# Kernel tuning notes

Measured on AMD Instinct MI355X. Metric: run time of the kernel, lower is better.

## Reference

```python
import jax, jax.numpy as jnp
import numpy as np

IMG = 512; P = 16; C = 3; DIM = 512; DEPTH = 2; HEADS = 8; HD = DIM // HEADS
MLP = 2048; W = 64; NCLS = 1000; B = 8
NPATCH = (IMG // P) ** 2          # 1024
N0 = NPATCH + 1                    # 1025 tokens incl CLS
PAD = (-N0) % (2 * W)              # pad to multiple of 2w (sliding_chunks)
N = N0 + PAD                       # 1152


def _ln(x, w, b):
    m = x.mean(-1, keepdims=True)
    v = jnp.mean((x - m) ** 2, -1, keepdims=True)
    return (x - m) * jax.lax.rsqrt(v + 1e-5) * w + b


def _heads(t):
    b, n, _ = t.shape
    return t.reshape(b, n, HEADS, HD).transpose(0, 2, 1, 3)  # b h n d


def _attn(x, mask, wq, bq, wk, bk, wv, bv, wqg, bqg, wkg, bkg, wvg, bvg):
    b, n, _ = x.shape
    sc = 1.0 / np.sqrt(HD)
    q = _heads(x @ wq + bq) * sc
    k = _heads(x @ wk + bk)
    v = _heads(x @ wv + bv)
    nc = n // W
    qc = q.reshape(b, HEADS, nc, W, HD)

    def chunk3(t):  # gather prev/self/next chunk of keys/values: b h nc 3W d
        tc = t.reshape(b, HEADS, nc, W, HD)
        z = jnp.zeros_like(tc[:, :, :1])
        prev = jnp.concatenate([z, tc[:, :, :-1]], 2)
        nxt = jnp.concatenate([tc[:, :, 1:], z], 2)
        return jnp.concatenate([prev, tc, nxt], 3)

    k3, v3 = chunk3(k), chunk3(v)
    band = jnp.einsum('bhcqd,bhckd->bhcqk', qc, k3)  # b h nc W 3W
    qi = jnp.arange(W)[:, None]
    kk = jnp.arange(3 * W)[None, :]
    rel_ok = jnp.abs(kk - W - qi) <= W               # exact +-w band
    kglob = jnp.arange(nc)[:, None, None] * W + (kk - W)[None]  # nc 1 3W
    in_rng = (kglob >= 0) & (kglob < n)
    kmask = mask[jnp.clip(kglob, 0, n - 1)]
    # keep only real local keys: exclude pad (0) and global (2, handled by gcol)
    keep = rel_ok[None] & in_rng & (kmask == 1.0)    # nc W 3W
    band = jnp.where(keep[None, None], band, -1e9)
    gcol = jnp.einsum('bhnd,bhd->bhn', q, k[:, :, 0])  # attend to global CLS key
    scores = jnp.concatenate([gcol[..., None], band.reshape(b, HEADS, n, 3 * W)], -1)
    a = jax.nn.softmax(scores, -1)                   # b h n (1+3W)
    out = jnp.einsum('bhcqk,bhckd->bhcqd', a[..., 1:].reshape(b, HEADS, nc, W, 3 * W), v3)
    out = out.reshape(b, HEADS, n, HD) + a[..., 0:1] * v[:, :, 0:1]
    # global CLS row attends to everything with its own projections
    qg0 = ((x[:, 0] @ wqg + bqg) * sc).reshape(b, HEADS, HD)
    kg = _heads(x @ wkg + bkg)
    vg = _heads(x @ wvg + bvg)
    gs = jnp.where(mask[None, None] > 0, jnp.einsum('bhd,bhnd->bhn', qg0, kg), -1e9)
    gout = jnp.einsum('bhn,bhnd->bhd', jax.nn.softmax(gs, -1), vg)
    out = out.at[:, :, 0].set(gout)
    return out.transpose(0, 2, 1, 3).reshape(b, n, DIM)


def setup_inputs():
    key = jax.random.key(0)
    ks = iter(jax.random.split(key, 20))

    def w(shape, s=0.02):
        return jax.random.normal(next(ks), shape, jnp.float32) * s

    return {
        'img': jax.random.normal(next(ks), (B, C, IMG, IMG), jnp.float32),
        'patch_w': w((P * P * C, DIM)), 'patch_b': jnp.zeros((DIM,), jnp.float32),
        'cls_tok': jax.random.uniform(next(ks), (1, 1, DIM), jnp.float32),
        'pos_emb': w((1, N0, DIM), 1.0),
        'ln1_w': jnp.ones((DEPTH, DIM), jnp.float32), 'ln1_b': jnp.zeros((DEPTH, DIM), jnp.float32),
        'wq': w((DEPTH, DIM, DIM)), 'bq': jnp.zeros((DEPTH, DIM), jnp.float32),
        'wk': w((DEPTH, DIM, DIM)), 'bk': jnp.zeros((DEPTH, DIM), jnp.float32),
        'wv': w((DEPTH, DIM, DIM)), 'bv': jnp.zeros((DEPTH, DIM), jnp.float32),
        'wqg': w((DEPTH, DIM, DIM)), 'bqg': jnp.zeros((DEPTH, DIM), jnp.float32),
        'wkg': w((DEPTH, DIM, DIM)), 'bkg': jnp.zeros((DEPTH, DIM), jnp.float32),
        'wvg': w((DEPTH, DIM, DIM)), 'bvg': jnp.zeros((DEPTH, DIM), jnp.float32),
        'ln2_w': jnp.ones((DEPTH, DIM), jnp.float32), 'ln2_b': jnp.zeros((DEPTH, DIM), jnp.float32),
        'w1': w((DEPTH, DIM, MLP)), 'b1': jnp.zeros((DEPTH, MLP), jnp.float32),
        'w2': w((DEPTH, MLP, DIM)), 'b2': jnp.zeros((DEPTH, DIM), jnp.float32),
        'head_ln_w': jnp.ones((DIM,), jnp.float32), 'head_ln_b': jnp.zeros((DIM,), jnp.float32),
        'head_w': w((DIM, NCLS)), 'head_b': jnp.zeros((NCLS,), jnp.float32),
    }


def reference(img, patch_w, patch_b, cls_tok, pos_emb, ln1_w, ln1_b, wq, bq, wk, bk,
              wv, bv, wqg, bqg, wkg, bkg, wvg, bvg, ln2_w, ln2_b, w1, b1, w2, b2,
              head_ln_w, head_ln_b, head_w, head_b):
    b = img.shape[0]
    hh = IMG // P
    # b c (h p1) (w p2) -> b (h w) (p1 p2 c)
    x = img.reshape(b, C, hh, P, hh, P).transpose(0, 2, 4, 3, 5, 1).reshape(b, hh * hh, P * P * C)
    x = x @ patch_w + patch_b
    x = jnp.concatenate([jnp.broadcast_to(cls_tok, (b, 1, DIM)), x], 1) + pos_emb
    x = jnp.pad(x, ((0, 0), (0, PAD), (0, 0)))
    mask = jnp.zeros((N,), jnp.float32).at[:N0].set(1.0).at[0].set(2.0)
    for i in range(DEPTH):
        x = x + _attn(_ln(x, ln1_w[i], ln1_b[i]), mask,
                      wq[i], bq[i], wk[i], bk[i], wv[i], bv[i],
                      wqg[i], bqg[i], wkg[i], bkg[i], wvg[i], bvg[i])
        h = jax.nn.gelu(_ln(x, ln2_w[i], ln2_b[i]) @ w1[i] + b1[i], approximate=False)
        x = x + h @ w2[i] + b2[i]
    cls = x[:, 0]  # pool='cls'
    return _ln(cls, head_ln_w, head_ln_b) @ head_w + head_b
```

## Files before the change

kernel.cpp:

```cpp
#include <hip/hip_runtime.h>
#include <hip/hip_bf16.h>
#include <math.h>

typedef __hip_bfloat16 bf16;
typedef float f32x4 __attribute__((ext_vector_type(4)));
typedef short s16x8 __attribute__((ext_vector_type(8)));
typedef unsigned int u32;

#define NB 8
#define NROW 1025
#define MTOT (NB*NROW)
#define DIMD 512
#define NHEAD 8
#define HD 64
#define MLPD 2048
#define QKVN 2560
#define JSTR 1032

__device__ __forceinline__ float b2f(short u) {
    return __builtin_bit_cast(float, (u32)(unsigned short)u << 16);
}
__device__ __forceinline__ unsigned short f2bfbits(float f) {
    __hip_bfloat16 h = __float2bfloat16(f);
    return __builtin_bit_cast(unsigned short, h);
}
__device__ __forceinline__ void g2lds16(const bf16* g, bf16* l) {
    __builtin_amdgcn_global_load_lds((const __attribute__((address_space(1))) u32*)g,
                                     (__attribute__((address_space(3))) u32*)l, 16, 0, 0);
}

__global__ __launch_bounds__(256) void transpose_cvt_L(
    const float* __restrict__ src, bf16* __restrict__ dst, int K, int N, float scale)
{
    __shared__ float t[32][33];
    const int z = blockIdx.z;
    const float* s = src + (size_t)z * K * N;
    bf16* d = dst + (size_t)z * N * K;
    const int n0 = blockIdx.x * 32, k0 = blockIdx.y * 32;
    const int tx = threadIdx.x, ty = threadIdx.y;
#pragma unroll
    for (int i = 0; i < 32; i += 8)
        t[ty + i][tx] = s[(long)(k0 + ty + i) * N + n0 + tx];
    __syncthreads();
#pragma unroll
    for (int i = 0; i < 32; i += 8)
        d[(long)(n0 + ty + i) * K + k0 + tx] = __float2bfloat16(t[tx][ty + i] * scale);
}

__global__ __launch_bounds__(256) void qkvw_t(
    const float* __restrict__ wq, const float* __restrict__ wk, const float* __restrict__ wv,
    const float* __restrict__ wkg, const float* __restrict__ wvg, bf16* __restrict__ qkvT)
{
    __shared__ float t[32][33];
    const int z = blockIdx.z, L = z / 5, s = z % 5;
    const float* srcs[5] = {wq, wk, wv, wkg, wvg};
    const float* src = srcs[s] + (size_t)L * DIMD * DIMD;
    bf16* dst = qkvT + ((size_t)L * QKVN + s * DIMD) * DIMD;
    const float scale = (s == 0) ? 0.125f : 1.f;
    const int n0 = blockIdx.x * 32, k0 = blockIdx.y * 32;
    const int tx = threadIdx.x, ty = threadIdx.y;
#pragma unroll
    for (int i = 0; i < 32; i += 8)
        t[ty + i][tx] = src[(long)(k0 + ty + i) * DIMD + n0 + tx];
    __syncthreads();
#pragma unroll
    for (int i = 0; i < 32; i += 8)
        dst[(long)(n0 + ty + i) * DIMD + k0 + tx] = __float2bfloat16(t[tx][ty + i] * scale);
}

__global__ __launch_bounds__(256) void build_bias(
    const float* __restrict__ bq, const float* __restrict__ bk, const float* __restrict__ bv,
    const float* __restrict__ bkg, const float* __restrict__ bvg, float* __restrict__ outb)
{
    int idx = blockIdx.x * 256 + threadIdx.x;
    if (idx >= 2 * QKVN) return;
    int L = idx / QKVN, c = idx % QKVN;
    int sec = c >> 9, d = c & 511;
    const float* src = (sec == 0) ? bq : (sec == 1) ? bk : (sec == 2) ? bv : (sec == 3) ? bkg : bvg;
    float v = src[L * DIMD + d];
    if (sec == 0) v *= 0.125f;
    outb[idx] = v;
}

__global__ __launch_bounds__(256) void im2col(
    const float* __restrict__ img, bf16* __restrict__ A)
{
    long idx = (long)blockIdx.x * 256 + threadIdx.x;
    if (idx >= (long)NB * 3 * 512 * 128) return;
    int ww4 = idx & 127;
    int hh  = (int)((idx >> 7) & 511);
    long rem = idx >> 16;
    int c = (int)(rem % 3), b = (int)(rem / 3);
    int w = ww4 * 4;
    const float4 pix = *(const float4*)(img + (((long)(b * 3 + c) * 512 + hh) * 512 + w));
    int ph = hh >> 4, py = hh & 15;
    int pw = w >> 4, px0 = w & 15;
    long arow = (long)b * 1024 + ph * 32 + pw;
    long abase = arow * 768 + (py * 16) * 3 + c;
    A[abase + (px0 + 0) * 3] = __float2bfloat16(pix.x);
    A[abase + (px0 + 1) * 3] = __float2bfloat16(pix.y);
    A[abase + (px0 + 2) * 3] = __float2bfloat16(pix.z);
    A[abase + (px0 + 3) * 3] = __float2bfloat16(pix.w);
}

__global__ __launch_bounds__(256) void assemble(
    const float* __restrict__ po, const float* __restrict__ cls,
    const float* __restrict__ pos, float* __restrict__ x)
{
    long idx = (long)blockIdx.x * 256 + threadIdx.x;
    if (idx >= (long)NB * NROW * DIMD) return;
    int d = (int)(idx & 511);
    long rem = idx >> 9;
    int n = (int)(rem % NROW), b = (int)(rem / NROW);
    float v;
    if (n == 0) v = cls[d] + pos[d];
    else        v = po[((long)b * 1024 + (n - 1)) * DIMD + d] + pos[(long)n * DIMD + d];
    x[idx] = v;
}

__global__ __launch_bounds__(256) void ln_fwd(
    const float* __restrict__ x, const float* __restrict__ w,
    const float* __restrict__ bb, bf16* __restrict__ y, int Mrows)
{
    const int row = blockIdx.x * 4 + (threadIdx.x >> 6);
    if (row >= Mrows) return;
    const int lane = threadIdx.x & 63;
    const float* xr = x + (long)row * DIMD + lane * 8;
    float4 a = *(const float4*)xr;
    float4 b4 = *(const float4*)(xr + 4);
    float s  = a.x + a.y + a.z + a.w + b4.x + b4.y + b4.z + b4.w;
    float sq = a.x*a.x + a.y*a.y + a.z*a.z + a.w*a.w + b4.x*b4.x + b4.y*b4.y + b4.z*b4.z + b4.w*b4.w;
#pragma unroll
    for (int o = 32; o; o >>= 1) { s += __shfl_xor(s, o); sq += __shfl_xor(sq, o); }
    float mean = s * (1.f / 512.f);
    float rstd = rsqrtf(sq * (1.f / 512.f) - mean * mean + 1e-5f);
    bf16* yr = y + (long)row * DIMD + lane * 8;
    const float* wp = w + lane * 8;
    const float* bp = bb + lane * 8;
    float vals[8] = {a.x, a.y, a.z, a.w, b4.x, b4.y, b4.z, b4.w};
#pragma unroll
    for (int u = 0; u < 8; ++u)
        yr[u] = __float2bfloat16((vals[u] - mean) * rstd * wp[u] + bp[u]);
}

template<int EPI>
__global__ __launch_bounds__(256) void gemm128(
    const bf16* __restrict__ A, const bf16* __restrict__ Bt,
    const float* __restrict__ bias,
    float* __restrict__ Cf, bf16* __restrict__ Cb,
    int M, int N, int K)
{
    __shared__ bf16 aL[2][128 * 32];
    __shared__ bf16 bL[2][128 * 32];
    const int tid = threadIdx.x, lane = tid & 63, w = tid >> 6;
    const int m0 = blockIdx.y * 128, n0 = blockIdx.x * 128;
    const int wm = w >> 1, wn = w & 1;
    f32x4 acc[4][4] = {};
    const int nk = K >> 5;
    const int lrow = lane >> 2, lk = (lane & 3) * 8;

#define STAGE(buf, kt) do {                                                       \
        _Pragma("unroll")                                                         \
        for (int i = 0; i < 2; ++i) {                                             \
            const int chunk = i * 4 + w;                                          \
            const int row = chunk * 16 + lrow;                                    \
            long ar = m0 + row; if (ar >= M) ar = M - 1;                          \
            g2lds16(A  + ar * (long)K + (long)(kt) * 32 + lk, &aL[buf][chunk*512]);\
            g2lds16(Bt + (long)(n0 + row) * K + (long)(kt) * 32 + lk, &bL[buf][chunk*512]);\
        } } while (0)

    STAGE(0, 0);
    __syncthreads();
    int cur = 0;
    const int abase = (wm * 64 + (lane & 15)) * 32 + (lane >> 4) * 8;
    const int bbase = (wn * 64 + (lane & 15)) * 32 + (lane >> 4) * 8;
    for (int kt = 0; kt < nk; ++kt) {
        if (kt + 1 < nk) STAGE(cur ^ 1, kt + 1);
        s16x8 af[4], bf_[4];
#pragma unroll
        for (int mi = 0; mi < 4; ++mi) af[mi]  = *(const s16x8*)(&aL[cur][abase + mi * 512]);
#pragma unroll
        for (int ni = 0; ni < 4; ++ni) bf_[ni] = *(const s16x8*)(&bL[cur][bbase + ni * 512]);
#pragma unroll
        for (int mi = 0; mi < 4; ++mi)
#pragma unroll
            for (int ni = 0; ni < 4; ++ni)
                acc[mi][ni] = __builtin_amdgcn_mfma_f32_16x16x32_bf16(af[mi], bf_[ni], acc[mi][ni], 0, 0, 0);
        __syncthreads();
        cur ^= 1;
    }
#undef STAGE
    const int lr = (lane >> 4) * 4, lc = lane & 15;
#pragma unroll
    for (int mi = 0; mi < 4; ++mi) {
        const int gr0 = m0 + wm * 64 + mi * 16 + lr;
#pragma unroll
        for (int ni = 0; ni < 4; ++ni) {
            const int gc = n0 + wn * 64 + ni * 16 + lc;
            const float bv = bias[gc];
#pragma unroll
            for (int j = 0; j < 4; ++j) {
                const int gr = gr0 + j;
                if (gr < M) {
                    float v = acc[mi][ni][j] + bv;
                    if (EPI == 0) Cf[(long)gr * N + gc] = v;
                    else if (EPI == 1) Cb[(long)gr * N + gc] = __float2bfloat16(v);
                    else if (EPI == 2) {
                        float g = 0.5f * v * (1.f + erff(v * 0.70710678118f));
                        Cb[(long)gr * N + gc] = __float2bfloat16(g);
                    } else {
                        Cf[(long)gr * N + gc] += v;
                    }
                }
            }
        }
    }
}

__global__ __launch_bounds__(256) void transpose_v(
    const bf16* __restrict__ qkv, bf16* __restrict__ vT)
{
    __shared__ bf16 t[32][34];
    const int b = blockIdx.z;
    const int j0 = blockIdx.x * 32, d0 = blockIdx.y * 32;
    const int tx = threadIdx.x, ty = threadIdx.y;
#pragma unroll
    for (int i = 0; i < 32; i += 8) {
        int j = j0 + ty + i; if (j > 1024) j = 1024;
        t[ty + i][tx] = qkv[((long)b * NROW + j) * QKVN + 1024 + d0 + tx];
    }
    __syncthreads();
#pragma unroll
    for (int i = 0; i < 32; i += 8) {
        int j = j0 + tx;
        if (j <= 1024)
            vT[((long)b * 512 + d0 + ty + i) * JSTR + j] = t[tx][ty + i];
    }
}

__global__ __launch_bounds__(256) void band_attn_mfma(
    const bf16* __restrict__ qkv, const bf16* __restrict__ vT, float* __restrict__ x)
{
    __shared__ bf16 Kl[208 * 72];
    __shared__ bf16 Vt[64 * 192];
    __shared__ bf16 Pl[4 * 16 * 192];
    __shared__ float V0l[64];
    const int c = blockIdx.x, h = blockIdx.y, b = blockIdx.z;
    const int tid = threadIdx.x, lane = tid & 63, w = tid >> 6;
    const int qi0 = 1 + c * 64, jbase = qi0 - 64;
    const long rowb = (long)b * NROW;
    const int hoff = h * HD;

    for (int task = tid; task < 208 * 8; task += 256) {
        const int d8 = task & 7, r = task >> 3;
        s16x8 val = {};
        if (r <= 192) {
            int j = (r < 192) ? (jbase + r) : 0;
            j = j < 0 ? 0 : (j > 1024 ? 1024 : j);
            val = *(const s16x8*)(qkv + (rowb + j) * QKVN + 512 + hoff + d8 * 8);
        }
        *(s16x8*)(Kl + r * 72 + d8 * 8) = val;
    }
    for (int task = tid; task < 64 * 24; task += 256) {
        const int kc = task % 24, d = task / 24;
        int j0 = jbase + kc * 8;
        j0 = j0 < 0 ? 0 : (j0 > 1017 ? 1017 : j0);
        s16x8 v = *(const s16x8*)(vT + ((long)(b * 512 + hoff + d)) * JSTR + j0);
        const int bo = (d * 384 + kc * 16) ^ ((d & 7) << 4);
        *(s16x8*)((char*)Vt + bo) = v;
    }
    if (tid < 64) V0l[tid] = __bfloat162float(qkv[rowb * QKVN + 1024 + hoff + tid]);

    const int q = lane & 15, g = lane >> 4;
    const int qg = w * 16 + q;
    s16x8 qf0, qf1;
    {
        const bf16* qp = qkv + (rowb + qi0 + qg) * QKVN + hoff + g * 8;
        qf0 = *(const s16x8*)qp;
        qf1 = *(const s16x8*)(qp + 32);
    }
    __syncthreads();

    f32x4 sc[13] = {};
#pragma unroll
    for (int nt = 0; nt < 13; ++nt) {
        const bf16* kp = Kl + (nt * 16 + q) * 72 + g * 8;
        s16x8 k0 = *(const s16x8*)kp;
        s16x8 k1 = *(const s16x8*)(kp + 32);
        sc[nt] = __builtin_amdgcn_mfma_f32_16x16x32_bf16(k0, qf0, sc[nt], 0, 0, 0);
        sc[nt] = __builtin_amdgcn_mfma_f32_16x16x32_bf16(k1, qf1, sc[nt], 0, 0, 0);
    }

    const int lo_ = (qg > 1 - jbase) ? qg : 1 - jbase;
    const int hi_ = (qg + 128 < 1024 - jbase) ? qg + 128 : 1024 - jbase;
    float m = -1e30f;
#pragma unroll
    for (int nt = 0; nt < 12; ++nt)
#pragma unroll
        for (int j = 0; j < 4; ++j) {
            const int slot = nt * 16 + g * 4 + j;
            float s = (slot >= lo_ && slot <= hi_) ? sc[nt][j] : -1e9f;
            sc[nt][j] = s;
            m = fmaxf(m, s);
        }
#pragma unroll
    for (int j = 0; j < 4; ++j) {
        float s = (g == 0 && j == 0) ? sc[12][j] : -1e9f;
        sc[12][j] = s;
        m = fmaxf(m, s);
    }
    m = fmaxf(m, __shfl_xor(m, 16));
    m = fmaxf(m, __shfl_xor(m, 32));
    float sum = 0.f;
#pragma unroll
    for (int nt = 0; nt < 13; ++nt)
#pragma unroll
        for (int j = 0; j < 4; ++j) {
            float p = __expf(sc[nt][j] - m);
            sc[nt][j] = p;
            sum += p;
        }
    sum += __shfl_xor(sum, 16);
    sum += __shfl_xor(sum, 32);
    const float inv = 1.f / sum;
    const float a0 = __shfl(sc[12][0], q);

    char* plw = (char*)Pl + w * 6144;
#pragma unroll
    for (int nt = 0; nt < 12; ++nt) {
        u32 lo2 = (u32)f2bfbits(sc[nt][0]) | ((u32)f2bfbits(sc[nt][1]) << 16);
        u32 hi2 = (u32)f2bfbits(sc[nt][2]) | ((u32)f2bfbits(sc[nt][3]) << 16);
        const int bo = (q * 384 + (nt * 16 + g * 4) * 2) ^ ((q & 7) << 4);
        *(uint2*)(plw + bo) = make_uint2(lo2, hi2);
    }
    __syncthreads();

    f32x4 ac[4] = {};
#pragma unroll
    for (int ks = 0; ks < 6; ++ks) {
        const int pbo = (q * 384 + (ks * 32 + g * 8) * 2) ^ ((q & 7) << 4);
        s16x8 pf = *(const s16x8*)(plw + pbo);
#pragma unroll
        for (int mt = 0; mt < 4; ++mt) {
            const int d = mt * 16 + q;
            const int vbo = ((d * 192 + ks * 32 + g * 8) * 2) ^ ((d & 7) << 4);
            s16x8 vf = *(const s16x8*)((char*)Vt + vbo);
            ac[mt] = __builtin_amdgcn_mfma_f32_16x16x32_bf16(vf, pf, ac[mt], 0, 0, 0);
        }
    }

    float* xr = x + (rowb + qi0 + qg) * DIMD + hoff;
#pragma unroll
    for (int mt = 0; mt < 4; ++mt) {
        const int d0 = mt * 16 + g * 4;
        float4 prev = *(float4*)(xr + d0);
        prev.x += (ac[mt][0] + a0 * V0l[d0 + 0]) * inv;
        prev.y += (ac[mt][1] + a0 * V0l[d0 + 1]) * inv;
        prev.z += (ac[mt][2] + a0 * V0l[d0 + 2]) * inv;
        prev.w += (ac[mt][3] + a0 * V0l[d0 + 3]) * inv;
        *(float4*)(xr + d0) = prev;
    }
}

__global__ __launch_bounds__(256) void qg_proj(
    const bf16* __restrict__ ybf, const float* __restrict__ wqg,
    const float* __restrict__ bqg, float* __restrict__ qg_all)
{
    __shared__ float y0[512];
    const int b = blockIdx.x, tid = threadIdx.x;
    const long rowb = (long)b * NROW;
    for (int d = tid; d < 512; d += 256) y0[d] = __bfloat162float(ybf[rowb * DIMD + d]);
    __syncthreads();
    const int c = blockIdx.y * 256 + tid;
    float a = 0.f;
#pragma unroll 8
    for (int kk = 0; kk < 512; ++kk) a += y0[kk] * wqg[(long)kk * DIMD + c];
    qg_all[b * DIMD + c] = (a + bqg[c]) * 0.125f;
}

__global__ __launch_bounds__(256) void glob_av(
    const float* __restrict__ qg_all, const bf16* __restrict__ qkv, float* __restrict__ x)
{
    __shared__ float qgs[64];
    __shared__ float red[256];
    __shared__ float P[1025];
    const int hh = blockIdx.x, b = blockIdx.y;
    const int tid = threadIdx.x;
    const long rowb = (long)b * NROW;
    const int hoff = hh * HD;
    if (tid < 64) qgs[tid] = qg_all[b * DIMD + hoff + tid];
    __syncthreads();
    const int dd = tid & 63, part = tid >> 6;
    for (int j = tid; j < 1025; j += 256) {
        const bf16* kr = qkv + (rowb + j) * QKVN + 1536 + hoff;
        float s = 0.f;
#pragma unroll
        for (int c8 = 0; c8 < 8; ++c8) {
            s16x8 kv = *(const s16x8*)(kr + c8 * 8);
#pragma unroll
            for (int e = 0; e < 8; ++e) s += qgs[c8 * 8 + e] * b2f(kv[e]);
        }
        P[j] = s;
    }
    __syncthreads();
    float lm = -1e30f;
    for (int j = tid; j < 1025; j += 256) lm = fmaxf(lm, P[j]);
    red[tid] = lm; __syncthreads();
    for (int st = 128; st; st >>= 1) { if (tid < st) red[tid] = fmaxf(red[tid], red[tid + st]); __syncthreads(); }
    const float mx = red[0]; __syncthreads();
    float ls = 0.f;
    for (int j = tid; j < 1025; j += 256) { float e = __expf(P[j] - mx); P[j] = e; ls += e; }
    red[tid] = ls; __syncthreads();
    for (int st = 128; st; st >>= 1) { if (tid < st) red[tid] += red[tid + st]; __syncthreads(); }
    const float inv = 1.f / red[0];
    __syncthreads();
    float acc = 0.f;
#pragma unroll 4
    for (int j = part; j < 1025; j += 4)
        acc += P[j] * __bfloat162float(qkv[(rowb + j) * QKVN + 2048 + hoff + dd]);
    red[tid] = acc;
    __syncthreads();
    if (part == 0)
        x[rowb * DIMD + hoff + dd] += (red[dd] + red[64 + dd] + red[128 + dd] + red[192 + dd]) * inv;
}

__global__ __launch_bounds__(512) void lncls(
    const float* __restrict__ x, const float* __restrict__ lw,
    const float* __restrict__ lb, float* __restrict__ out)
{
    const int b = threadIdx.x >> 6, lane = threadIdx.x & 63;
    const int d0 = lane * 8;
    const float* xr = x + (long)b * NROW * DIMD + d0;
    float4 a = *(const float4*)xr;
    float4 b4 = *(const float4*)(xr + 4);
    float s  = a.x + a.y + a.z + a.w + b4.x + b4.y + b4.z + b4.w;
    float sq = a.x*a.x + a.y*a.y + a.z*a.z + a.w*a.w + b4.x*b4.x + b4.y*b4.y + b4.z*b4.z + b4.w*b4.w;
#pragma unroll
    for (int o = 32; o; o >>= 1) { s += __shfl_xor(s, o); sq += __shfl_xor(sq, o); }
    const float mean = s * (1.f / 512.f);
    const float rstd = rsqrtf(sq * (1.f / 512.f) - mean * mean + 1e-5f);
    float vals[8] = {a.x, a.y, a.z, a.w, b4.x, b4.y, b4.z, b4.w};
#pragma unroll
    for (int u = 0; u < 8; ++u)
        out[b * DIMD + d0 + u] = (vals[u] - mean) * rstd * lw[d0 + u] + lb[d0 + u];
}

__global__ __launch_bounds__(128) void head_gemv(
    const float* __restrict__ lnc, const float* __restrict__ hw,
    const float* __restrict__ hb, float* __restrict__ out)
{
    const int idx = blockIdx.x * 128 + threadIdx.x;
    if (idx >= NB * 1000) return;
    const int b = idx / 1000, cc = idx - b * 1000;
    const float* lr = lnc + b * DIMD;
    float a = hb[cc];
#pragma unroll 8
    for (int kk = 0; kk < 512; ++kk) a += lr[kk] * hw[(long)kk * 1000 + cc];
    out[idx] = a;
}

extern "C" void kernel_launch(void* const* d_in, const int* in_sizes, int n_in,
                              void* d_out, int out_size, void* d_ws, size_t ws_size,
                              hipStream_t stream)
{
    const float* img     = (const float*)d_in[0];
    const float* patch_w = (const float*)d_in[1];
    const float* patch_b = (const float*)d_in[2];
    const float* cls_tok = (const float*)d_in[3];
    const float* pos_emb = (const float*)d_in[4];
    const float* ln1_w   = (const float*)d_in[5];
    const float* ln1_b   = (const float*)d_in[6];
    const float* wq  = (const float*)d_in[7];
    const float* bq  = (const float*)d_in[8];
    const float* wk  = (const float*)d_in[9];
    const float* bk  = (const float*)d_in[10];
    const float* wv  = (const float*)d_in[11];
    const float* bv  = (const float*)d_in[12];
    const float* wqg = (const float*)d_in[13];
    const float* bqg = (const float*)d_in[14];
    const float* wkg = (const float*)d_in[15];
    const float* bkg = (const float*)d_in[16];
    const float* wvg = (const float*)d_in[17];
    const float* bvg = (const float*)d_in[18];
    const float* ln2_w = (const float*)d_in[19];
    const float* ln2_b = (const float*)d_in[20];
    const float* w1 = (const float*)d_in[21];
    const float* b1 = (const float*)d_in[22];
    const float* w2 = (const float*)d_in[23];
    const float* b2 = (const float*)d_in[24];
    const float* hlw = (const float*)d_in[25];
    const float* hlb = (const float*)d_in[26];
    const float* hw  = (const float*)d_in[27];
    const float* hb  = (const float*)d_in[28];

    char* wsb = (char*)d_ws;
    size_t o = 0;
    auto carve = [&](size_t n) { size_t r = o; o += (n + 255) & ~(size_t)255; return r; };
    float* x    = (float*)(wsb + carve((size_t)MTOT * DIMD * 4));
    bf16*  ybf  = (bf16*) (wsb + carve((size_t)MTOT * DIMD * 2));
    bf16*  qkv  = (bf16*) (wsb + carve((size_t)MTOT * QKVN * 2));
    bf16*  hbuf = (bf16*) (wsb + carve((size_t)MTOT * MLPD * 2));
    float* pout = (float*)(wsb + carve((size_t)8192 * DIMD * 4));
    bf16*  acol = (bf16*) (wsb + carve((size_t)8192 * 768 * 2));
    bf16*  pwt  = (bf16*) (wsb + carve((size_t)512 * 768 * 2));
    bf16*  qkvT = (bf16*) (wsb + carve((size_t)2 * QKVN * DIMD * 2));
    bf16*  w1t  = (bf16*) (wsb + carve((size_t)2 * MLPD * DIMD * 2));
    bf16*  w2t  = (bf16*) (wsb + carve((size_t)2 * DIMD * MLPD * 2));
    float* catb = (float*)(wsb + carve((size_t)2 * QKVN * 4));
    float* qg_all = (float*)(wsb + carve((size_t)NB * DIMD * 4));
    float* lnc    = (float*)(wsb + carve((size_t)NB * DIMD * 4));
    bf16*  vT   = (bf16*)pout;
    (void)ws_size; (void)in_sizes; (void)n_in; (void)out_size;

    dim3 tb(32, 8);
    transpose_cvt_L<<<dim3(16, 24, 1), tb, 0, stream>>>(patch_w, pwt, 768, 512, 1.f);
    qkvw_t<<<dim3(16, 16, 10), tb, 0, stream>>>(wq, wk, wv, wkg, wvg, qkvT);
    transpose_cvt_L<<<dim3(64, 16, 2), tb, 0, stream>>>(w1, w1t, DIMD, MLPD, 1.f);
    transpose_cvt_L<<<dim3(16, 64, 2), tb, 0, stream>>>(w2, w2t, MLPD, DIMD, 1.f);
    build_bias<<<20, 256, 0, stream>>>(bq, bk, bv, bkg, bvg, catb);

    im2col<<<6144, 256, 0, stream>>>(img, acol);
    gemm128<0><<<dim3(4, 64), 256, 0, stream>>>(acol, pwt, patch_b, pout, nullptr, 8192, 512, 768);
    assemble<<<16400, 256, 0, stream>>>(pout, cls_tok, pos_emb, x);

    for (int L = 0; L < 2; ++L) {
        ln_fwd<<<2050, 256, 0, stream>>>(x, ln1_w + L * DIMD, ln1_b + L * DIMD, ybf, MTOT);
        gemm128<1><<<dim3(QKVN/128, 65), 256, 0, stream>>>(
            ybf, qkvT + (size_t)L * QKVN * DIMD, catb + L * QKVN, nullptr, qkv, MTOT, QKVN, DIMD);
        transpose_v<<<dim3(33, 16, NB), tb, 0, stream>>>(qkv, vT);
        band_attn_mfma<<<dim3(16, NHEAD, NB), 256, 0, stream>>>(qkv, vT, x);
        qg_proj<<<dim3(NB, 2), 256, 0, stream>>>(
            ybf, wqg + (size_t)L * DIMD * DIMD, bqg + L * DIMD, qg_all);
        glob_av<<<dim3(NHEAD, NB), 256, 0, stream>>>(qg_all, qkv, x);
        ln_fwd<<<2050, 256, 0, stream>>>(x, ln2_w + L * DIMD, ln2_b + L * DIMD, ybf, MTOT);
        gemm128<2><<<dim3(MLPD/128, 65), 256, 0, stream>>>(
            ybf, w1t + (size_t)L * MLPD * DIMD, b1 + L * MLPD, nullptr, hbuf, MTOT, MLPD, DIMD);
        gemm128<3><<<dim3(DIMD/128, 65), 256, 0, stream>>>(
            hbuf, w2t + (size_t)L * DIMD * MLPD, b2 + L * DIMD, x, nullptr, MTOT, DIMD, MLPD);
    }
    lncls<<<1, 512, 0, stream>>>(x, hlw, hlb, lnc);
    head_gemv<<<63, 128, 0, stream>>>(lnc, hw, hb, (float*)d_out);
}
```

Measured before the change: 590.2 us.

## Widen GEMM K-tile to 64 with XOR-swizzled LDS layout

Result: no change. 590.2 us (-0.0%).

```diff
diff --git a/kernel.cpp b/kernel.cpp
--- a/kernel.cpp
+++ b/kernel.cpp
@@ -150,42 +150,52 @@
     float* __restrict__ Cf, bf16* __restrict__ Cb,
     int M, int N, int K)
 {
-    __shared__ bf16 aL[2][128 * 32];
-    __shared__ bf16 bL[2][128 * 32];
+    __shared__ bf16 aL[2][128 * 64];
+    __shared__ bf16 bL[2][128 * 64];
     const int tid = threadIdx.x, lane = tid & 63, w = tid >> 6;
     const int m0 = blockIdx.y * 128, n0 = blockIdx.x * 128;
     const int wm = w >> 1, wn = w & 1;
     f32x4 acc[4][4] = {};
-    const int nk = K >> 5;
-    const int lrow = lane >> 2, lk = (lane & 3) * 8;
-
-#define STAGE(buf, kt) do {                                                       \
-        _Pragma("unroll")                                                         \
-        for (int i = 0; i < 2; ++i) {                                             \
-            const int chunk = i * 4 + w;                                          \
-            const int row = chunk * 16 + lrow;                                    \
-            long ar = m0 + row; if (ar >= M) ar = M - 1;                          \
-            g2lds16(A  + ar * (long)K + (long)(kt) * 32 + lk, &aL[buf][chunk*512]);\
-            g2lds16(Bt + (long)(n0 + row) * K + (long)(kt) * 32 + lk, &bL[buf][chunk*512]);\
+    const int nk = K >> 6;
+    const int srow = lane >> 3;
+    const int scol = ((lane & 7) ^ srow) * 8;
+
+#define STAGE(buf, kt) do {                                                        \
+        _Pragma("unroll")                                                          \
+        for (int i = 0; i < 4; ++i) {                                              \
+            const int rb = i * 32 + w * 8;                                         \
+            long ar = m0 + rb + srow; if (ar >= M) ar = M - 1;                     \
+            g2lds16(A  + ar * (long)K + (long)(kt) * 64 + scol, &aL[buf][rb * 64]);\
+            g2lds16(Bt + (long)(n0 + rb + srow) * K + (long)(kt) * 64 + scol,      \
+                    &bL[buf][rb * 64]);                                            \
         } } while (0)
 
     STAGE(0, 0);
     __syncthreads();
     int cur = 0;
-    const int abase = (wm * 64 + (lane & 15)) * 32 + (lane >> 4) * 8;
-    const int bbase = (wn * 64 + (lane & 15)) * 32 + (lane >> 4) * 8;
+    const int fr = lane & 15;
+    const int lc0 = lane >> 4;
+    const int px = lane & 7;
+    const int arow_b = (wm * 64 + fr) << 7;
+    const int brow_b = (wn * 64 + fr) << 7;
     for (int kt = 0; kt < nk; ++kt) {
         if (kt + 1 < nk) STAGE(cur ^ 1, kt + 1);
-        s16x8 af[4], bf_[4];
-#pragma unroll
-        for (int mi = 0; mi < 4; ++mi) af[mi]  = *(const s16x8*)(&aL[cur][abase + mi * 512]);
-#pragma unroll
-        for (int ni = 0; ni < 4; ++ni) bf_[ni] = *(const s16x8*)(&bL[cur][bbase + ni * 512]);
-#pragma unroll
-        for (int mi = 0; mi < 4; ++mi)
-#pragma unroll
-            for (int ni = 0; ni < 4; ++ni)
-                acc[mi][ni] = __builtin_amdgcn_mfma_f32_16x16x32_bf16(af[mi], bf_[ni], acc[mi][ni], 0, 0, 0);
+        const char* aP = (const char*)&aL[cur][0];
+        const char* bP = (const char*)&bL[cur][0];
+#pragma unroll
+        for (int ksub = 0; ksub < 2; ++ksub) {
+            const int cb = ((ksub * 4 + lc0) ^ px) << 4;
+            s16x8 af[4], bf_[4];
+#pragma unroll
+            for (int mi = 0; mi < 4; ++mi) af[mi]  = *(const s16x8*)(aP + arow_b + mi * 2048 + cb);
+#pragma unroll
+            for (int ni = 0; ni < 4; ++ni) bf_[ni] = *(const s16x8*)(bP + brow_b + ni * 2048 + cb);
+#pragma unroll
+            for (int mi = 0; mi < 4; ++mi)
+#pragma unroll
+                for (int ni = 0; ni < 4; ++ni)
+                    acc[mi][ni] = __builtin_amdgcn_mfma_f32_16x16x32_bf16(af[mi], bf_[ni], acc[mi][ni], 0, 0, 0);
+        }
         __syncthreads();
         cur ^= 1;
     }
```
